# Kernel tuning notes

Hardware: AMD Instinct MI355X
Metric: run time of the kernel (lower is better)

## Reference

```python
import jax, jax.numpy as jnp
import numpy as np

B, C, S = 32, 64, 112
RATIO = 8
EPS = 1e-5


def conv1x1(x, w, b):
    # 1x1 conv == channel-mixing matmul. x:[B,C,H,W], w:[O,C], b:[O]
    return jnp.einsum('oc,bchw->bohw', w, x) + b[None, :, None, None]


def dwconv(x, w, b):
    # grouped 1x1 conv with groups=C: per-channel scale + bias
    return x * w[None, :, None, None] + b[None, :, None, None]


def bn(x, g, b):
    # BatchNorm2d in training mode: batch stats over (N,H,W), biased var
    m = x.mean((0, 2, 3), keepdims=True)
    v = x.var((0, 2, 3), keepdims=True)
    return (x - m) * jax.lax.rsqrt(v + EPS) * g[None, :, None, None] + b[None, :, None, None]


def avgpool(x, k):
    # nn.AvgPool2d(k): kernel k, stride k, VALID (floor) padding
    s = jax.lax.reduce_window(x, 0.0, jax.lax.add, (1, 1, k, k), (1, 1, k, k), 'VALID')
    return s / float(k * k)


def setup_inputs() -> dict:
    key = jax.random.key(0)
    ks = jax.random.split(key, 20)
    C2, H = 2 * C, (2 * C) // RATIO

    def n(k, shape, s=0.02):
        return jax.random.normal(k, shape, jnp.float32) * s

    return {
        'rgb': jax.random.normal(ks[0], (B, C, S, S), jnp.float32),
        'fre': jax.random.normal(ks[1], (B, C, S, S), jnp.float32),
        'wq_fad': n(ks[2], (C, C)), 'bq_fad': jnp.zeros((C,), jnp.float32),
        'wq_lfs': n(ks[3], (C, C)), 'bq_lfs': jnp.zeros((C,), jnp.float32),
        'wk_fad': n(ks[4], (C, C)), 'bk_fad': jnp.zeros((C,), jnp.float32),
        'wk_lfs': n(ks[5], (C, C)), 'bk_lfs': jnp.zeros((C,), jnp.float32),
        'fad_gamma': n(ks[6], (1,), 1.0), 'lfs_gamma': n(ks[7], (1,), 1.0),
        'fad_cw': n(ks[8], (C,), 1.0), 'fad_cb': jnp.zeros((C,), jnp.float32),
        'fad_bg': jnp.ones((C,), jnp.float32), 'fad_bb': jnp.zeros((C,), jnp.float32),
        'lfs_cw': n(ks[9], (C,), 1.0), 'lfs_cb': jnp.zeros((C,), jnp.float32),
        'lfs_bg': jnp.ones((C,), jnp.float32), 'lfs_bb': jnp.zeros((C,), jnp.float32),
        'lin1_w': n(ks[10], (3,), 0.3), 'lin2_w': n(ks[11], (3,), 0.3),
        'mlp_w1': n(ks[12], (H, C2)), 'mlp_w2': n(ks[13], (C2, H)),
        'rgb_cw': n(ks[14], (C,), 1.0), 'rgb_cb': jnp.zeros((C,), jnp.float32),
        'rgb_bg': jnp.ones((C,), jnp.float32), 'rgb_bb': jnp.zeros((C,), jnp.float32),
        'fre_cw': n(ks[15], (C,), 1.0), 'fre_cb': jnp.zeros((C,), jnp.float32),
        'fre_bg': jnp.ones((C,), jnp.float32), 'fre_bb': jnp.zeros((C,), jnp.float32),
    }


def reference(rgb, fre, wq_fad, bq_fad, wq_lfs, bq_lfs, wk_fad, bk_fad, wk_lfs, bk_lfs,
              fad_gamma, lfs_gamma, fad_cw, fad_cb, fad_bg, fad_bb,
              lfs_cw, lfs_cb, lfs_bg, lfs_bb, lin1_w, lin2_w, mlp_w1, mlp_w2,
              rgb_cw, rgb_cb, rgb_bg, rgb_bb, fre_cw, fre_cb, fre_bg, fre_bb):
    Bn, Cn, Sz, _ = rgb.shape
    # ---- MixBlock: cross attention over folded (B*C) batch ----
    qF = conv1x1(rgb, wq_fad, bq_fad).reshape(Bn * Cn, Sz, Sz)
    qL = conv1x1(fre, wq_lfs, bq_lfs).reshape(Bn * Cn, Sz, Sz)
    Mq = jnp.concatenate([qF, qL], axis=2)          # [BC, S, 2S]
    kF = conv1x1(rgb, wk_fad, bk_fad).reshape(Bn * Cn, Sz, Sz).transpose(0, 2, 1)
    kL = conv1x1(fre, wk_lfs, bk_lfs).reshape(Bn * Cn, Sz, Sz).transpose(0, 2, 1)
    Mk = jnp.concatenate([kF, kL], axis=1)          # [BC, 2S, S]
    attn = jax.nn.softmax(jnp.matmul(Mq, Mk), axis=-1).reshape(Bn, Cn, Sz, Sz)
    att_lfs = fre * attn * (jax.nn.sigmoid(lfs_gamma) * 2.0 - 1.0)
    y_fad = rgb + bn(dwconv(att_lfs, fad_cw, fad_cb), fad_bg, fad_bb)
    att_fad = rgb * attn * (jax.nn.sigmoid(fad_gamma) * 2.0 - 1.0)
    y_lfs = fre + bn(dwconv(att_fad, lfs_cw, lfs_cb), lfs_bg, lfs_bb)
    # ---- MSCA on concatenated channels ----
    x = jnp.concatenate([y_fad, y_lfs], axis=1)     # [B, 2C, S, S]
    avgs, maxs = [], []
    for k in (3, 5, 7):
        m = avgpool(x, k)
        avgs.append(m.mean((2, 3)))
        maxs.append(m.max((2, 3)))
    a_p = jnp.stack(avgs, -1) @ lin1_w              # [B, 2C]
    m_p = jnp.stack(maxs, -1) @ lin2_w

    def mlp(v):
        h = jax.nn.relu(jnp.einsum('rc,bc->br', mlp_w1, v))
        return jnp.einsum('cr,br->bc', mlp_w2, h)

    ca = jax.nn.sigmoid(mlp(a_p) + mlp(m_p))        # [B, 2C]
    r_c = ca[:, :Cn, None, None]
    f_c = ca[:, Cn:, None, None]
    rgb_out = y_fad + bn(dwconv(r_c * y_fad, rgb_cw, rgb_cb), rgb_bg, rgb_bb)
    fre_out = y_lfs + bn(dwconv(f_c * y_lfs, fre_cw, fre_cb), fre_bg, fre_bb)
    return (rgb_out, fre_out)
```

## Files before the change

### kernel.cpp

```cpp
#include <hip/hip_runtime.h>
#include <hip/hip_bf16.h>
#include <stdint.h>

#define NE 25690112ull
#define PP 12544
#define SS 112
#define EPSV 1e-5f

typedef __attribute__((ext_vector_type(8))) short short8v;
typedef __attribute__((ext_vector_type(4))) float float4v;

__device__ __forceinline__ unsigned short f2bf(float x){
  union { float f; uint32_t u; } v; v.f = x;
  uint32_t r = (v.u + 0x7fffu + ((v.u >> 16) & 1u)) >> 16;
  return (unsigned short)r;
}
__device__ __forceinline__ float bf2f(unsigned short u){ return __uint_as_float(((uint32_t)u) << 16); }

__global__ __launch_bounds__(256) void k1_conv(
    const float* __restrict__ rgb, const float* __restrict__ fre,
    const float* __restrict__ wq_fad, const float* __restrict__ bq_fad,
    const float* __restrict__ wk_fad, const float* __restrict__ bk_fad,
    const float* __restrict__ wq_lfs, const float* __restrict__ bq_lfs,
    const float* __restrict__ wk_lfs, const float* __restrict__ bk_lfs,
    unsigned short* __restrict__ qF, unsigned short* __restrict__ kF,
    unsigned short* __restrict__ qL, unsigned short* __restrict__ kL,
    unsigned short* __restrict__ rgbb, unsigned short* __restrict__ freb)
{
  const int bx = blockIdx.x, b = blockIdx.y, z = blockIdx.z;
  const float* X  = z ? fre : rgb;
  const float* Wq = z ? wq_lfs : wq_fad;
  const float* Bq = z ? bq_lfs : bq_fad;
  const float* Wk = z ? wk_lfs : wk_fad;
  const float* Bk = z ? bk_lfs : bk_fad;
  unsigned short* Oq = z ? qL : qF;
  unsigned short* Ok = z ? kL : kF;
  unsigned short* Xb = z ? freb : rgbb;

  __shared__ __align__(16) unsigned short xs[256 * 64];

  const int tid = threadIdx.x, lane = tid & 63, w = tid >> 6;
  const int lc = lane & 15, l4 = lane >> 4;

  const int p0 = bx*256;
  const size_t xbase = (size_t)b * 64 * PP;
  const int c0 = (tid & 15) * 4;
  const int pq = (tid >> 4) * 4;
  #pragma unroll
  for (int itp = 0; itp < 4; ++itp){
    const int p = itp*64 + pq;
    float4 xr[4];
    #pragma unroll
    for (int k = 0; k < 4; ++k)
      xr[k] = *(const float4*)(X + xbase + (size_t)(c0+k)*PP + p0 + p);
    #pragma unroll
    for (int k = 0; k < 4; ++k){
      ushort4 s;
      s.x = f2bf(xr[k].x); s.y = f2bf(xr[k].y); s.z = f2bf(xr[k].z); s.w = f2bf(xr[k].w);
      *(ushort4*)(Xb + xbase + (size_t)(c0+k)*PP + p0 + p) = s;
    }
    float vals[4][4];
    #pragma unroll
    for (int k = 0; k < 4; ++k){ vals[k][0]=xr[k].x; vals[k][1]=xr[k].y; vals[k][2]=xr[k].z; vals[k][3]=xr[k].w; }
    #pragma unroll
    for (int j = 0; j < 4; ++j){
      ushort4 t;
      t.x = f2bf(vals[0][j]); t.y = f2bf(vals[1][j]); t.z = f2bf(vals[2][j]); t.w = f2bf(vals[3][j]);
      uint32_t byteS = (uint32_t)((p+j)*128 + c0*2) ^ (uint32_t)(((p+j) & 7) << 4);
      *(ushort4*)((char*)xs + byteS) = t;
    }
  }
  __syncthreads();

  short8v afr[4][2];
  #pragma unroll
  for (int t = 0; t < 4; ++t){
    const int row = (t*4 + w)*16 + lc;
    const uint32_t rbase = (uint32_t)(row*128);
    const uint32_t sw = (uint32_t)((row & 7) << 4);
    afr[t][0] = *(const short8v*)((const char*)xs + ((rbase + l4*16) ^ sw));
    afr[t][1] = *(const short8v*)((const char*)xs + ((rbase + 64 + l4*16) ^ sw));
  }
  __syncthreads();

  #pragma unroll
  for (int arr = 0; arr < 2; ++arr){
    const float* W = arr ? Wk : Wq;
    const float* Bi = arr ? Bk : Bq;
    unsigned short* O = arr ? Ok : Oq;
    short8v wf[4][2];
    float bias[4];
    #pragma unroll
    for (int ot = 0; ot < 4; ++ot){
      bias[ot] = Bi[ot*16 + lc];
      #pragma unroll
      for (int ks = 0; ks < 2; ++ks){
        const int base = (ot*16 + lc)*64 + ks*32 + l4*8;
        const float4 q0 = *(const float4*)(W + base);
        const float4 q1 = *(const float4*)(W + base + 4);
        short8v v;
        v[0]=(short)f2bf(q0.x); v[1]=(short)f2bf(q0.y); v[2]=(short)f2bf(q0.z); v[3]=(short)f2bf(q0.w);
        v[4]=(short)f2bf(q1.x); v[5]=(short)f2bf(q1.y); v[6]=(short)f2bf(q1.z); v[7]=(short)f2bf(q1.w);
        wf[ot][ks] = v;
      }
    }
    #pragma unroll
    for (int t = 0; t < 4; ++t){
      const int pt = (t*4 + w)*16;
      #pragma unroll
      for (int ot = 0; ot < 4; ++ot){
        float4v acc = (float4v){bias[ot], bias[ot], bias[ot], bias[ot]};
        acc = __builtin_amdgcn_mfma_f32_16x16x32_bf16(afr[t][0], wf[ot][0], acc, 0, 0, 0);
        acc = __builtin_amdgcn_mfma_f32_16x16x32_bf16(afr[t][1], wf[ot][1], acc, 0, 0, 0);
        ushort4 u;
        u.x = f2bf(acc[0]); u.y = f2bf(acc[1]); u.z = f2bf(acc[2]); u.w = f2bf(acc[3]);
        const int o = ot*16 + lc;
        uint32_t byteS = (uint32_t)(o*512 + (pt + l4*4)*2) ^ (uint32_t)((o & 7) << 4);
        *(ushort4*)((char*)xs + byteS) = u;
      }
    }
    __syncthreads();
    for (int i = tid; i < 2048; i += 256){
      const int o = i >> 5, s = i & 31;
      uint32_t byteS = (uint32_t)(o*512 + s*16) ^ (uint32_t)((o & 7) << 4);
      short8v v = *(const short8v*)((const char*)xs + byteS);
      *(short8v*)(O + ((size_t)b*64 + o)*PP + p0 + s*8) = v;
    }
    __syncthreads();
  }
}

__global__ __launch_bounds__(448) void k2_attn(
    unsigned short* __restrict__ qF, const unsigned short* __restrict__ qL,
    const unsigned short* __restrict__ kF, const unsigned short* __restrict__ kL,
    const unsigned short* __restrict__ rgbb, const unsigned short* __restrict__ freb,
    const float* __restrict__ fad_gamma, const float* __restrict__ lfs_gamma,
    float* __restrict__ stats)
{
  const int bc = blockIdx.x, c = bc & 63;
  const size_t plane = (size_t)bc * PP;
  __shared__ __align__(16) unsigned short ksF[112][128];
  __shared__ __align__(16) unsigned short ksL[112][128];
  const int tid = threadIdx.x, lane = tid & 63, w = tid >> 6;
  const int l4 = lane >> 4, lc = lane & 15;

  const uint32_t* kFu = (const uint32_t*)kF + plane/2;
  const uint32_t* kLu = (const uint32_t*)kL + plane/2;
  for (int i = tid; i < 7168; i += 448){
    int row = i >> 6, wd = i & 63;
    uint32_t vF = (wd < 56) ? kFu[row*56 + wd] : 0u;
    uint32_t vL = (wd < 56) ? kLu[row*56 + wd] : 0u;
    uint32_t byteS = (uint32_t)((row << 8) | (wd << 2)) ^ (uint32_t)((row & 7) << 4);
    *(uint32_t*)((char*)&ksF[0][0] + byteS) = vF;
    *(uint32_t*)((char*)&ksL[0][0] + byteS) = vL;
  }
  __syncthreads();

  float4v acc[7];
  #pragma unroll
  for (int ct = 0; ct < 7; ++ct) acc[ct] = (float4v)0.f;

  const unsigned short* qFp = qF + plane;
  const unsigned short* qLp = qL + plane;
  const int qrow = w*16 + lc;
  #pragma unroll
  for (int ks = 0; ks < 4; ++ks){
    short8v aF = (short8v)(short)0, aL = (short8v)(short)0;
    const int joff = ks*32 + l4*8;
    if ((ks < 3) || (l4 < 2)){
      aF = *(const short8v*)(qFp + qrow*SS + joff);
      aL = *(const short8v*)(qLp + qrow*SS + joff);
    }
    #pragma unroll
    for (int ct = 0; ct < 7; ++ct){
      uint32_t byteS = (uint32_t)((ct*16 + lc)*256 + ks*64 + l4*16) ^ (uint32_t)((lc & 7) << 4);
      short8v bF = *(const short8v*)((const char*)&ksF[0][0] + byteS);
      short8v bL = *(const short8v*)((const char*)&ksL[0][0] + byteS);
      acc[ct] = __builtin_amdgcn_mfma_f32_16x16x32_bf16(aF, bF, acc[ct], 0, 0, 0);
      acc[ct] = __builtin_amdgcn_mfma_f32_16x16x32_bf16(aL, bL, acc[ct], 0, 0, 0);
    }
  }

  const float sF = 2.f/(1.f + __expf(-fad_gamma[0])) - 1.f;
  const float sL = 2.f/(1.f + __expf(-lfs_gamma[0])) - 1.f;
  float ls1 = 0.f, lq1 = 0.f, ls2 = 0.f, lq2 = 0.f;
  unsigned short* attnP = qF + plane;

  #pragma unroll
  for (int r = 0; r < 4; ++r){
    const int i = w*16 + l4*4 + r;
    float v[7];
    #pragma unroll
    for (int ct = 0; ct < 7; ++ct) v[ct] = acc[ct][r];
    float m = fmaxf(fmaxf(fmaxf(v[0],v[1]),fmaxf(v[2],v[3])), fmaxf(fmaxf(v[4],v[5]),v[6]));
    #pragma unroll
    for (int off = 8; off; off >>= 1) m = fmaxf(m, __shfl_xor(m, off, 64));
    float e[7]; float s = 0.f;
    #pragma unroll
    for (int ct = 0; ct < 7; ++ct){ e[ct] = __expf(v[ct] - m); s += e[ct]; }
    #pragma unroll
    for (int off = 8; off; off >>= 1) s += __shfl_xor(s, off, 64);
    const float inv = 1.f / s;
    const size_t rb = plane + (size_t)i * SS;
    #pragma unroll
    for (int ct = 0; ct < 7; ++ct){
      const int col = ct*16 + lc;
      unsigned short ab = f2bf(e[ct] * inv);
      attnP[(size_t)i*SS + col] = ab;
      float a  = bf2f(ab);
      float frv = bf2f(freb[rb + col]), rgv = bf2f(rgbb[rb + col]);
      float v1 = frv * a * sL, v2 = rgv * a * sF;
      ls1 += v1; lq1 += v1*v1; ls2 += v2; lq2 += v2*v2;
    }
  }
  #pragma unroll
  for (int off = 32; off; off >>= 1){
    ls1 += __shfl_xor(ls1, off, 64);
    lq1 += __shfl_xor(lq1, off, 64);
    ls2 += __shfl_xor(ls2, off, 64);
    lq2 += __shfl_xor(lq2, off, 64);
  }
  if (lane == 0){
    atomicAdd(&stats[c],       ls1);
    atomicAdd(&stats[64 + c],  lq1);
    atomicAdd(&stats[128 + c], ls2);
    atomicAdd(&stats[192 + c], lq2);
  }
}

__global__ void k3_affine1(const float* __restrict__ stats,
    const float* __restrict__ fad_cw, const float* __restrict__ fad_bg, const float* __restrict__ fad_bb,
    const float* __restrict__ lfs_cw, const float* __restrict__ lfs_bg, const float* __restrict__ lfs_bb,
    float* __restrict__ AB)
{
  int c = threadIdx.x;
  if (c >= 64) return;
  const float n = 401408.f;
  {
    float m1 = stats[c]/n, v1 = stats[64+c]/n - (stats[c]/n)*(stats[c]/n);
    float cw = fad_cw[c], g = fad_bg[c];
    float rs = rsqrtf(cw*cw*v1 + EPSV);
    AB[c]      = cw*rs*g;
    AB[64 + c] = -cw*m1*rs*g + fad_bb[c];
  }
  {
    float m2 = stats[128+c]/n, v2 = stats[192+c]/n - (stats[128+c]/n)*(stats[128+c]/n);
    float cw = lfs_cw[c], g = lfs_bg[c];
    float rs = rsqrtf(cw*cw*v2 + EPSV);
    AB[128 + c] = cw*rs*g;
    AB[192 + c] = -cw*m2*rs*g + lfs_bb[c];
  }
}

__global__ __launch_bounds__(512) void k4_fuse(
    const unsigned short* __restrict__ attn,
    const unsigned short* __restrict__ rgbb, const unsigned short* __restrict__ freb,
    const float* __restrict__ AB1,
    const float* __restrict__ fad_gamma, const float* __restrict__ lfs_gamma,
    unsigned short* __restrict__ ybf, unsigned short* __restrict__ ybl,
    float* __restrict__ avgstat, float* __restrict__ maxstat,
    float4* __restrict__ planeStats)
{
  const int bc = blockIdx.x, b = bc >> 6, c = bc & 63;
  const size_t plane = (size_t)bc * PP;
  __shared__ unsigned short ys[2][112][113];
  __shared__ float redA[8][4];
  __shared__ float redS[8], redM[8];
  const int tid = threadIdx.x, lane = tid & 63, w = tid >> 6;
  const float sF = 2.f/(1.f + __expf(-fad_gamma[0])) - 1.f;
  const float sL = 2.f/(1.f + __expf(-lfs_gamma[0])) - 1.f;
  const float A1 = AB1[c], B1 = AB1[64+c], A2 = AB1[128+c], B2 = AB1[192+c];
  float s0 = 0.f, q0 = 0.f, s1 = 0.f, q1 = 0.f;

  for (int i4 = tid; i4 < 3136; i4 += 512){
    ushort4 av = *(const ushort4*)(attn + plane + (size_t)i4*4);
    ushort4 rg = *(const ushort4*)(rgbb + plane + (size_t)i4*4);
    ushort4 fr = *(const ushort4*)(freb + plane + (size_t)i4*4);
    float aa[4] = {bf2f(av.x), bf2f(av.y), bf2f(av.z), bf2f(av.w)};
    float rr[4] = {bf2f(rg.x), bf2f(rg.y), bf2f(rg.z), bf2f(rg.w)};
    float ff[4] = {bf2f(fr.x), bf2f(fr.y), bf2f(fr.z), bf2f(fr.w)};
    float y0[4], y1[4];
    ushort4 o0, o1;
    unsigned short* p0 = &o0.x; unsigned short* p1 = &o1.x;
    #pragma unroll
    for (int j = 0; j < 4; ++j){
      float t1 = ff[j]*aa[j]*sL;
      float t2 = rr[j]*aa[j]*sF;
      y0[j] = rr[j] + A1*t1 + B1;
      y1[j] = ff[j] + A2*t2 + B2;
      s0 += y0[j]; q0 += y0[j]*y0[j];
      s1 += y1[j]; q1 += y1[j]*y1[j];
      p0[j] = f2bf(y0[j]);
      p1[j] = f2bf(y1[j]);
    }
    *(ushort4*)(ybf + plane + (size_t)i4*4) = o0;
    *(ushort4*)(ybl + plane + (size_t)i4*4) = o1;
    int r = i4 / 28, c0 = (i4 % 28) * 4;
    #pragma unroll
    for (int j = 0; j < 4; ++j){
      ys[0][r][c0+j] = p0[j];
      ys[1][r][c0+j] = p1[j];
    }
  }
  #pragma unroll
  for (int off = 32; off; off >>= 1){
    s0 += __shfl_xor(s0, off, 64); q0 += __shfl_xor(q0, off, 64);
    s1 += __shfl_xor(s1, off, 64); q1 += __shfl_xor(q1, off, 64);
  }
  if (lane == 0){ redA[w][0] = s0; redA[w][1] = q0; redA[w][2] = s1; redA[w][3] = q1; }
  __syncthreads();
  if (tid == 0){
    float a0=0,a1=0,a2=0,a3=0;
    for (int i = 0; i < 8; ++i){ a0+=redA[i][0]; a1+=redA[i][1]; a2+=redA[i][2]; a3+=redA[i][3]; }
    float4 ps = {a0,a1,a2,a3};
    planeStats[bc] = ps;
  }
  __syncthreads();

  const int kk[3] = {3,5,7};
  const int gg[3] = {37,22,16};
  for (int pl = 0; pl < 2; ++pl){
    const int cc = pl*64 + c;
    for (int ki = 0; ki < 3; ++ki){
      const int k = kk[ki], g = gg[ki];
      float sumAll = 0.f, mx = -3.0e38f;
      for (int win = tid; win < g*g; win += 512){
        int wy = win / g, wx = win % g;
        float s = 0.f;
        for (int dy = 0; dy < k; ++dy)
          for (int dx = 0; dx < k; ++dx)
            s += bf2f(ys[pl][wy*k+dy][wx*k+dx]);
        sumAll += s; mx = fmaxf(mx, s);
      }
      #pragma unroll
      for (int off = 32; off; off >>= 1){
        sumAll += __shfl_xor(sumAll, off, 64);
        mx = fmaxf(mx, __shfl_xor(mx, off, 64));
      }
      if (lane == 0){ redS[w] = sumAll; redM[w] = mx; }
      __syncthreads();
      if (tid == 0){
        float st = 0.f, mt = -3.0e38f;
        for (int i = 0; i < 8; ++i){ st += redS[i]; mt = fmaxf(mt, redM[i]); }
        int idx = (b*128 + cc)*3 + ki;
        avgstat[idx] = st / (float)(k*k*g*g);
        maxstat[idx] = mt / (float)(k*k);
      }
      __syncthreads();
    }
  }
}

__global__ void k6_mlp(const float* __restrict__ avgstat, const float* __restrict__ maxstat,
    const float* __restrict__ lin1, const float* __restrict__ lin2,
    const float* __restrict__ w1, const float* __restrict__ w2,
    float* __restrict__ ca)
{
  const int b = blockIdx.x, tid = threadIdx.x;
  __shared__ float sa[128], sm[128], hA[16], hM[16];
  int idx = (b*128 + tid)*3;
  sa[tid] = avgstat[idx]*lin1[0] + avgstat[idx+1]*lin1[1] + avgstat[idx+2]*lin1[2];
  sm[tid] = maxstat[idx]*lin2[0] + maxstat[idx+1]*lin2[1] + maxstat[idx+2]*lin2[2];
  __syncthreads();
  if (tid < 16){
    float ha = 0.f, hm = 0.f;
    for (int c2 = 0; c2 < 128; ++c2){
      ha += w1[tid*128 + c2]*sa[c2];
      hm += w1[tid*128 + c2]*sm[c2];
    }
    hA[tid] = fmaxf(ha, 0.f); hM[tid] = fmaxf(hm, 0.f);
  }
  __syncthreads();
  float o = 0.f;
  for (int r = 0; r < 16; ++r) o += w2[tid*16 + r]*(hA[r] + hM[r]);
  ca[b*128 + tid] = 1.f/(1.f + __expf(-o));
}

__global__ void k8_affineF(const float4* __restrict__ planeStats, const float* __restrict__ ca,
    const float* __restrict__ rgb_cw, const float* __restrict__ rgb_bg, const float* __restrict__ rgb_bb,
    const float* __restrict__ fre_cw, const float* __restrict__ fre_bg, const float* __restrict__ fre_bb,
    float* __restrict__ ABF)
{
  int t = threadIdx.x;
  if (t >= 128) return;
  int z = t >> 6, c = t & 63;
  float S = 0.f, Q = 0.f;
  for (int b = 0; b < 32; ++b){
    float4 ps = planeStats[b*64 + c];
    float sc = ca[b*128 + t];
    float sp = z ? ps.z : ps.x;
    float qp = z ? ps.w : ps.y;
    S += sc*sp; Q += sc*sc*qp;
  }
  const float n = 401408.f;
  float m = S/n, v = Q/n - m*m;
  float cw = z ? fre_cw[c] : rgb_cw[c];
  float g  = z ? fre_bg[c] : rgb_bg[c];
  float bb = z ? fre_bb[c] : rgb_bb[c];
  float rs = rsqrtf(cw*cw*v + EPSV);
  ABF[z*128 + c]      = cw*rs*g;
  ABF[z*128 + 64 + c] = -cw*m*rs*g + bb;
}

__global__ __launch_bounds__(256) void k9_out(
    const unsigned short* __restrict__ ybf, const unsigned short* __restrict__ ybl,
    const float* __restrict__ ca, const float* __restrict__ ABF,
    float* __restrict__ out)
{
  const int c = blockIdx.x, b = blockIdx.y, z = blockIdx.z;
  const size_t plane = ((size_t)b*64 + c)*PP;
  const unsigned short* y = z ? ybl : ybf;
  float* o = out + (z ? NE : 0) + plane;
  const float sc = ca[b*128 + z*64 + c];
  const float A = ABF[z*128 + c], Bv = ABF[z*128 + 64 + c];
  const float mul = 1.f + A*sc;
  for (int i8 = threadIdx.x; i8 < 1568; i8 += 256){
    short8v yv = *(const short8v*)(y + plane + (size_t)i8*8);
    float4 o0, o1;
    o0.x = bf2f((unsigned short)yv[0])*mul + Bv;
    o0.y = bf2f((unsigned short)yv[1])*mul + Bv;
    o0.z = bf2f((unsigned short)yv[2])*mul + Bv;
    o0.w = bf2f((unsigned short)yv[3])*mul + Bv;
    o1.x = bf2f((unsigned short)yv[4])*mul + Bv;
    o1.y = bf2f((unsigned short)yv[5])*mul + Bv;
    o1.z = bf2f((unsigned short)yv[6])*mul + Bv;
    o1.w = bf2f((unsigned short)yv[7])*mul + Bv;
    *(float4*)(&o[(size_t)i8*8])     = o0;
    *(float4*)(&o[(size_t)i8*8 + 4]) = o1;
  }
}

extern "C" void kernel_launch(void* const* d_in, const int* in_sizes, int n_in,
                              void* d_out, int out_size, void* d_ws, size_t ws_size,
                              hipStream_t stream)
{
  (void)in_sizes; (void)n_in; (void)out_size; (void)ws_size;
  const float* rgb      = (const float*)d_in[0];
  const float* fre      = (const float*)d_in[1];
  const float* wq_fad   = (const float*)d_in[2];
  const float* bq_fad   = (const float*)d_in[3];
  const float* wq_lfs   = (const float*)d_in[4];
  const float* bq_lfs   = (const float*)d_in[5];
  const float* wk_fad   = (const float*)d_in[6];
  const float* bk_fad   = (const float*)d_in[7];
  const float* wk_lfs   = (const float*)d_in[8];
  const float* bk_lfs   = (const float*)d_in[9];
  const float* fad_gamma= (const float*)d_in[10];
  const float* lfs_gamma= (const float*)d_in[11];
  const float* fad_cw   = (const float*)d_in[12];
  const float* fad_bg   = (const float*)d_in[14];
  const float* fad_bb   = (const float*)d_in[15];
  const float* lfs_cw   = (const float*)d_in[16];
  const float* lfs_bg   = (const float*)d_in[18];
  const float* lfs_bb   = (const float*)d_in[19];
  const float* lin1_w   = (const float*)d_in[20];
  const float* lin2_w   = (const float*)d_in[21];
  const float* mlp_w1   = (const float*)d_in[22];
  const float* mlp_w2   = (const float*)d_in[23];
  const float* rgb_cw   = (const float*)d_in[24];
  const float* rgb_bg   = (const float*)d_in[26];
  const float* rgb_bb   = (const float*)d_in[27];
  const float* fre_cw   = (const float*)d_in[28];
  const float* fre_bg   = (const float*)d_in[30];
  const float* fre_bb   = (const float*)d_in[31];

  char* ws = (char*)d_ws;
  unsigned short* qF = (unsigned short*)(ws);
  unsigned short* qL = (unsigned short*)(ws + 2*NE);
  unsigned short* kF = (unsigned short*)(ws + 4*NE);
  unsigned short* kL = (unsigned short*)(ws + 6*NE);
  float* sbase = (float*)(ws + 8*NE);
  float* stats      = sbase;
  float* AB1        = sbase + 256;
  float* avgstat    = sbase + 512;
  float* maxstat    = sbase + 12800;
  float* ca         = sbase + 25088;
  float* ABF        = sbase + 29184;
  float4* planeStats= (float4*)(sbase + 29440);
  unsigned short* rgbb = (unsigned short*)d_out;
  unsigned short* freb = (unsigned short*)d_out + NE;

  hipMemsetAsync(stats, 0, 256*sizeof(float), stream);

  k1_conv<<<dim3(49,32,2), dim3(256), 0, stream>>>(rgb, fre,
      wq_fad, bq_fad, wk_fad, bk_fad, wq_lfs, bq_lfs, wk_lfs, bk_lfs,
      qF, kF, qL, kL, rgbb, freb);
  k2_attn<<<dim3(2048), dim3(448), 0, stream>>>(qF, qL, kF, kL,
      rgbb, freb, fad_gamma, lfs_gamma, stats);
  k3_affine1<<<dim3(1), dim3(64), 0, stream>>>(stats,
      fad_cw, fad_bg, fad_bb, lfs_cw, lfs_bg, lfs_bb, AB1);
  k4_fuse<<<dim3(2048), dim3(512), 0, stream>>>((const unsigned short*)qF,
      rgbb, freb, AB1, fad_gamma, lfs_gamma, kF, kL, avgstat, maxstat, planeStats);
  k6_mlp<<<dim3(32), dim3(128), 0, stream>>>(avgstat, maxstat,
      lin1_w, lin2_w, mlp_w1, mlp_w2, ca);
  k8_affineF<<<dim3(1), dim3(128), 0, stream>>>(planeStats, ca,
      rgb_cw, rgb_bg, rgb_bb, fre_cw, fre_bg, fre_bb, ABF);
  k9_out<<<dim3(64,32,2), dim3(256), 0, stream>>>(kF, kL, ca, ABF,
      (float*)d_out);
}
```

Baseline: 446.3 us.

## Coalesce input load in conv kernel and stage softmax output through LDS

The conv kernel now loads each channel row contiguously per wave (coalesced float4 along pixels) and stores it channel-major in padded LDS, then gathers the MFMA A-fragments with scalar 16-bit LDS reads. The attention kernel writes softmax rows into shared memory first, then copies the whole plane to global with vectorized ushort4 stores while reading fre/rgb bf16 in vectorized form for the BN statistics. This targets uncoalesced global access at the cost of more LDS traffic, extra barriers, and scalar LDS gathers.

```diff
diff --git a/kernel.cpp b/kernel.cpp
--- a/kernel.cpp
+++ b/kernel.cpp
@@ -37,49 +37,37 @@
   unsigned short* Ok = z ? kL : kF;
   unsigned short* Xb = z ? freb : rgbb;
 
-  __shared__ __align__(16) unsigned short xs[256 * 64];
+  __shared__ __align__(16) unsigned short xs[64 * 260];
 
   const int tid = threadIdx.x, lane = tid & 63, w = tid >> 6;
   const int lc = lane & 15, l4 = lane >> 4;
 
   const int p0 = bx*256;
   const size_t xbase = (size_t)b * 64 * PP;
-  const int c0 = (tid & 15) * 4;
-  const int pq = (tid >> 4) * 4;
-  #pragma unroll
-  for (int itp = 0; itp < 4; ++itp){
-    const int p = itp*64 + pq;
-    float4 xr[4];
-    #pragma unroll
-    for (int k = 0; k < 4; ++k)
-      xr[k] = *(const float4*)(X + xbase + (size_t)(c0+k)*PP + p0 + p);
-    #pragma unroll
-    for (int k = 0; k < 4; ++k){
-      ushort4 s;
-      s.x = f2bf(xr[k].x); s.y = f2bf(xr[k].y); s.z = f2bf(xr[k].z); s.w = f2bf(xr[k].w);
-      *(ushort4*)(Xb + xbase + (size_t)(c0+k)*PP + p0 + p) = s;
-    }
-    float vals[4][4];
-    #pragma unroll
-    for (int k = 0; k < 4; ++k){ vals[k][0]=xr[k].x; vals[k][1]=xr[k].y; vals[k][2]=xr[k].z; vals[k][3]=xr[k].w; }
-    #pragma unroll
-    for (int j = 0; j < 4; ++j){
-      ushort4 t;
-      t.x = f2bf(vals[0][j]); t.y = f2bf(vals[1][j]); t.z = f2bf(vals[2][j]); t.w = f2bf(vals[3][j]);
-      uint32_t byteS = (uint32_t)((p+j)*128 + c0*2) ^ (uint32_t)(((p+j) & 7) << 4);
-      *(ushort4*)((char*)xs + byteS) = t;
-    }
+  #pragma unroll
+  for (int i = 0; i < 16; ++i){
+    const int c = w*16 + i;
+    const size_t gof = xbase + (size_t)c*PP + p0 + lane*4;
+    float4 xv = *(const float4*)(X + gof);
+    ushort4 s;
+    s.x = f2bf(xv.x); s.y = f2bf(xv.y); s.z = f2bf(xv.z); s.w = f2bf(xv.w);
+    *(ushort4*)(Xb + gof) = s;
+    *(ushort4*)(&xs[c*260 + lane*4]) = s;
   }
   __syncthreads();
 
   short8v afr[4][2];
   #pragma unroll
   for (int t = 0; t < 4; ++t){
-    const int row = (t*4 + w)*16 + lc;
-    const uint32_t rbase = (uint32_t)(row*128);
-    const uint32_t sw = (uint32_t)((row & 7) << 4);
-    afr[t][0] = *(const short8v*)((const char*)xs + ((rbase + l4*16) ^ sw));
-    afr[t][1] = *(const short8v*)((const char*)xs + ((rbase + 64 + l4*16) ^ sw));
+    const int p = (t*4 + w)*16 + lc;
+    #pragma unroll
+    for (int ks = 0; ks < 2; ++ks){
+      short8v a;
+      #pragma unroll
+      for (int j = 0; j < 8; ++j)
+        a[j] = (short)xs[(ks*32 + l4*8 + j)*260 + p];
+      afr[t][ks] = a;
+    }
   }
   __syncthreads();
 
@@ -183,9 +171,10 @@
 
   const float sF = 2.f/(1.f + __expf(-fad_gamma[0])) - 1.f;
   const float sL = 2.f/(1.f + __expf(-lfs_gamma[0])) - 1.f;
-  float ls1 = 0.f, lq1 = 0.f, ls2 = 0.f, lq2 = 0.f;
   unsigned short* attnP = qF + plane;
-
+  unsigned short* alin = &ksF[0][0];
+
+  __syncthreads();
   #pragma unroll
   for (int r = 0; r < 4; ++r){
     const int i = w*16 + l4*4 + r;
@@ -201,15 +190,26 @@
     #pragma unroll
     for (int off = 8; off; off >>= 1) s += __shfl_xor(s, off, 64);
     const float inv = 1.f / s;
-    const size_t rb = plane + (size_t)i * SS;
-    #pragma unroll
-    for (int ct = 0; ct < 7; ++ct){
-      const int col = ct*16 + lc;
-      unsigned short ab = f2bf(e[ct] * inv);
-      attnP[(size_t)i*SS + col] = ab;
-      float a  = bf2f(ab);
-      float frv = bf2f(freb[rb + col]), rgv = bf2f(rgbb[rb + col]);
-      float v1 = frv * a * sL, v2 = rgv * a * sF;
+    #pragma unroll
+    for (int ct = 0; ct < 7; ++ct)
+      alin[i*SS + ct*16 + lc] = f2bf(e[ct] * inv);
+  }
+  __syncthreads();
+
+  float ls1 = 0.f, lq1 = 0.f, ls2 = 0.f, lq2 = 0.f;
+  for (int i4 = tid; i4 < 3136; i4 += 448){
+    ushort4 av = *(const ushort4*)(alin + i4*4);
+    *(ushort4*)(attnP + (size_t)i4*4) = av;
+    ushort4 fr = *(const ushort4*)(freb + plane + (size_t)i4*4);
+    ushort4 rg = *(const ushort4*)(rgbb + plane + (size_t)i4*4);
+    const unsigned short* ap = &av.x;
+    const unsigned short* fp = &fr.x;
+    const unsigned short* rp = &rg.x;
+    #pragma unroll
+    for (int j = 0; j < 4; ++j){
+      float a = bf2f(ap[j]);
+      float v1 = bf2f(fp[j]) * a * sL;
+      float v2 = bf2f(rp[j]) * a * sF;
       ls1 += v1; lq1 += v1*v1; ls2 += v2; lq2 += v2*v2;
     }
   }
```

Result: faster. 425.0 us (-4.8%).
